# Optimization experiments

Hardware: AMD Instinct MI355X
Metric: run time of the kernel (lower is better)

The kernel has to match this reference:

```python
import jax, jax.numpy as jnp
from jax import lax
import numpy as np

T, B, D = 24, 64, 1536
R, NUM_BLOCK = 5120, 5
NBN = R // NUM_BLOCK  # 1024 neurons per block
C = 100
THR_BASE = 0.5
REF_BASE = 0.5
Q0 = 0.8  # (100-20)/100 from wta_mem_update


@jax.custom_vjp
def spike_fn(v):
    # act_fun: heaviside forward, rectangular surrogate gradient
    return (v > 0).astype(v.dtype)

def _spike_fwd(v):
    return (v > 0).astype(v.dtype), v

def _spike_bwd(v, g):
    return (g * (jnp.abs(v) < 0.5).astype(g.dtype),)

spike_fn.defvjp(_spike_fwd, _spike_bwd)


def setup_inputs() -> dict:
    key = jax.random.key(0)
    ks = jax.random.split(key, 16)
    f32 = jnp.float32
    x = jax.random.normal(ks[0], (T, B, D), dtype=f32)
    Wp = jax.random.normal(ks[1], (R, D), dtype=f32) / np.sqrt(D)
    Wl = jax.random.normal(ks[2], (R, R), dtype=f32) / np.sqrt(R)
    Wm = jax.random.normal(ks[3], (C, R), dtype=f32) / np.sqrt(R)
    # adaptive LIF per-neuron parameters (as in __init__)
    decay = jax.random.uniform(ks[4], (R,), dtype=f32)
    thr_beta = 0.1 * jax.random.uniform(ks[5], (R,), dtype=f32)
    thr_decay = 0.5 * jax.random.uniform(ks[6], (R,), dtype=f32)
    ref_beta = 0.1 * jax.random.uniform(ks[7], (R,), dtype=f32)
    ref_decay = 0.5 * jax.random.uniform(ks[8], (R,), dtype=f32)
    cur_beta = 0.1 * jax.random.uniform(ks[9], (R,), dtype=f32)
    cur_decay = 0.5 * jax.random.uniform(ks[10], (R,), dtype=f32)
    # block-structured projection mask: [D, R] then transpose to weight layout [R, D]
    mask = np.zeros((D, R), dtype=np.float32)
    cum = np.cumsum([0, 512, 512, 256, 128])  # [0,512,1024,1280,1408]
    for i in range(len(cum) - 1):
        mask[cum[i]:cum[i + 1], NBN * i:NBN * (i + 1)] = 1.0
    proj_mask = jnp.asarray(mask.T)
    # sparse lateral mask: rand>0.8, no self-connection
    rng = np.random.RandomState(0)
    lat = (rng.rand(R, R) > 0.8).astype(np.float32)
    lat = lat * (1.0 - np.eye(R, dtype=np.float32))
    lat_mask = jnp.asarray(lat.T)
    return {
        "x": x, "ln_g": jnp.ones((D,), f32), "ln_b": jnp.zeros((D,), f32),
        "Wp": Wp, "bp": jnp.zeros((R,), f32), "Wl": Wl, "bl": jnp.zeros((R,), f32),
        "Wm": Wm, "bm": jnp.zeros((C,), f32),
        "decay": decay, "thr_beta": thr_beta, "thr_decay": thr_decay,
        "ref_beta": ref_beta, "ref_decay": ref_decay,
        "cur_beta": cur_beta, "cur_decay": cur_decay,
        "proj_mask": proj_mask, "lat_mask": lat_mask,
    }


def reference(x, ln_g, ln_b, Wp, bp, Wl, bl, Wm, bm,
              decay, thr_beta, thr_decay, ref_beta, ref_decay,
              cur_beta, cur_decay, proj_mask, lat_mask):
    Tn, Bn, Dn = x.shape
    Rn = Wp.shape[0]
    # parameter clamps done in forward of the torch module
    dec = jnp.clip(decay, 0.0, 1.0)
    thd = jnp.clip(thr_decay, 0.0, 1.0)
    rfd = jnp.clip(ref_decay, 0.0, 1.0)
    cud = jnp.clip(cur_decay, 0.0, 1.0)
    Wp_m = Wp * proj_mask       # masked feedforward projection
    Wl_m = Wl * lat_mask        # masked lateral recurrence
    # LayerNorm over fused multimodal features
    mu = x.mean(-1, keepdims=True)
    var = x.var(-1, keepdims=True)
    xn = (x - mu) * lax.rsqrt(var + 1e-5) * ln_g + ln_b
    # precompute feedforward drive for all steps: [T, B, R]
    drive = jnp.einsum('tbd,rd->tbr', xn, Wp_m) + bp

    def step(carry, dr_t):
        spike, mem, ttr, rtr, ctr, ssum = carry
        state = dr_t + spike @ Wl_m.T + bl
        thr = THR_BASE + thr_beta * ttr
        ref = REF_BASE + ref_beta * rtr
        cur = cur_beta * ctr
        mem = (mem - spike * ref) * dec + state + cur
        # WTA: quantile-threshold per group (torch row-major reshape [B, NBN, NUM_BLOCK])
        m3 = mem.reshape(Bn, NBN, NUM_BLOCK)
        nps = jnp.quantile(m3, Q0, axis=1, keepdims=True)
        mem = jax.nn.relu(m3 - nps).reshape(Bn, Rn)
        spk = spike_fn(mem - thr)
        ttr = ttr * thd + spk
        rtr = rtr * rfd + spk
        ctr = ctr * cud + spk
        return (spk, mem, ttr, rtr, ctr, ssum + spk), None

    z = jnp.zeros((Bn, Rn), x.dtype)
    (spk, mem, _, _, _, ssum), _ = lax.scan(step, (z, z, z, z, z, z), drive)
    # readout on time-averaged spike counts
    return (ssum / Tn) @ Wm.T + bm
```

## Files before the change

### kernel.cpp

```cpp
#include <hip/hip_runtime.h>
#include <math.h>

#define TSTEPS 24
#define BB 64
#define DD 1536
#define RR 5120
#define NB 5
#define CC 100
#define KS 2
#define WSCALE 67108864.0f

typedef int i32x4 __attribute__((ext_vector_type(4)));

__device__ __forceinline__ int q_to_r(int q) { return (q & 1023) * 5 + (q >> 10); }

__constant__ int KOFF[4] = {0, 512, 1024, 1280};
__constant__ int KLEN[4] = {512, 512, 256, 128};
__constant__ int PBASE[4] = {0, 524288, 1048576, 1310720};

__device__ __forceinline__ unsigned fkey(float f) {
  unsigned u = __float_as_uint(f);
  return u ^ (((unsigned)((int)u >> 31)) | 0x80000000u);
}
__device__ __forceinline__ float fkeyinv(unsigned k) {
  unsigned u = (k & 0x80000000u) ? (k ^ 0x80000000u) : ~k;
  return __uint_as_float(u);
}

__global__ __launch_bounds__(256) void k_zero(float* __restrict__ state,
                                              unsigned* __restrict__ spike_i8_u32) {
  size_t n = 6ull * BB * RR;
  size_t nb = (size_t)BB * RR / 4;
  size_t gi = (size_t)blockIdx.x * 256 + threadIdx.x;
  for (size_t i = gi; i < n; i += (size_t)gridDim.x * 256) state[i] = 0.0f;
  for (size_t i = gi; i < nb; i += (size_t)gridDim.x * 256) spike_i8_u32[i] = 0u;
}

__global__ __launch_bounds__(256) void k_prep_params(
    const float* __restrict__ bp, const float* __restrict__ bl,
    const float* __restrict__ dec, const float* __restrict__ tb,
    const float* __restrict__ td, const float* __restrict__ rb,
    const float* __restrict__ rd, const float* __restrict__ cb,
    const float* __restrict__ cd, float* __restrict__ P) {
  int q = blockIdx.x * 256 + threadIdx.x;
  if (q >= RR) return;
  int r = q_to_r(q);
  P[0 * RR + q] = bp[r] + bl[r];
  P[1 * RR + q] = fminf(fmaxf(dec[r], 0.f), 1.f);
  P[2 * RR + q] = tb[r];
  P[3 * RR + q] = fminf(fmaxf(td[r], 0.f), 1.f);
  P[4 * RR + q] = rb[r];
  P[5 * RR + q] = fminf(fmaxf(rd[r], 0.f), 1.f);
  P[6 * RR + q] = cb[r];
  P[7 * RR + q] = fminf(fmaxf(cd[r], 0.f), 1.f);
}

__global__ __launch_bounds__(256) void k_prep_wm(const float* __restrict__ Wm,
                                                 float* __restrict__ Wmp) {
  int c = blockIdx.x;
  for (int q = threadIdx.x; q < RR; q += 256)
    Wmp[(size_t)c * RR + q] = Wm[(size_t)c * RR + q_to_r(q)];
}

__global__ __launch_bounds__(256) void k_prep_wpb(const float* __restrict__ Wp,
                                                  const float* __restrict__ pm,
                                                  float* __restrict__ Wpb) {
  int r = blockIdx.x;
  int i = r >> 10;
  int koff = KOFF[i], klen = KLEN[i];
  const float* src = Wp + (size_t)r * DD + koff;
  const float* msk = pm + (size_t)r * DD + koff;
  float* dst = Wpb + PBASE[i] + (size_t)(r - (i << 10)) * klen;
  for (int k = threadIdx.x; k < klen; k += 256) dst[k] = src[k] * msk[k];
}

__global__ __launch_bounds__(256) void k_build_q4tab(const float* __restrict__ bp,
                                                     const float* __restrict__ bl,
                                                     int* __restrict__ qtab,
                                                     float* __restrict__ vtab) {
  for (int idx = threadIdx.x; idx < 1024; idx += 256) {
    int j, i;
    if (idx < 204) { j = 0; i = 820 + idx; }
    else { int e = idx - 204; j = 1 + e / 205; i = 819 + e % 205; }
    int r = i * 5 + j;
    qtab[idx] = j * 1024 + i;
    vtab[idx] = bp[r] + bl[r];
  }
}

__global__ __launch_bounds__(256) void k_build_wq_i8(const float* __restrict__ Wl,
                                                     const float* __restrict__ lmask,
                                                     signed char* __restrict__ Bd) {
  int qn = blockIdx.x;
  int rn = q_to_r(qn);
  const float4* wr = (const float4*)(Wl + (size_t)rn * RR);
  const float4* mr = (const float4*)(lmask + (size_t)rn * RR);
  size_t ob = (size_t)qn * RR;
  const size_t plane = (size_t)RR * RR;
  for (int v4 = threadIdx.x; v4 < RR / 4; v4 += 256) {
    float4 wv = wr[v4];
    float4 mv = mr[v4];
    float w[4] = {wv.x * mv.x, wv.y * mv.y, wv.z * mv.z, wv.w * mv.w};
    unsigned char o0[4], o1[4], o2[4];
#pragma unroll
    for (int c = 0; c < 4; c++) {
      int wi = (int)rintf(w[c] * WSCALE);
      int d0 = (int)(signed char)(wi & 0xFF);
      int rem = (wi - d0) >> 8;
      int d1 = (int)(signed char)(rem & 0xFF);
      rem = (rem - d1) >> 8;
      o0[c] = (unsigned char)d0;
      o1[c] = (unsigned char)d1;
      o2[c] = (unsigned char)(rem & 0xFF);
    }
    *(uchar4*)(Bd + ob + 4 * v4) = make_uchar4(o0[0], o0[1], o0[2], o0[3]);
    *(uchar4*)(Bd + plane + ob + 4 * v4) = make_uchar4(o1[0], o1[1], o1[2], o1[3]);
    *(uchar4*)(Bd + 2 * plane + ob + 4 * v4) = make_uchar4(o2[0], o2[1], o2[2], o2[3]);
  }
}

__global__ __launch_bounds__(256) void k_layernorm(const float* __restrict__ x,
                                                   const float* __restrict__ g,
                                                   const float* __restrict__ be,
                                                   float* __restrict__ xn) {
  __shared__ float red[4];
  int row = blockIdx.x;
  int tid = threadIdx.x;
  const float* xr = x + (size_t)row * DD;
  float v[6];
  float s = 0.f;
#pragma unroll
  for (int i = 0; i < 6; i++) { v[i] = xr[i * 256 + tid]; s += v[i]; }
  for (int o = 32; o > 0; o >>= 1) s += __shfl_down(s, o, 64);
  int wv = tid >> 6, lane = tid & 63;
  if (lane == 0) red[wv] = s;
  __syncthreads();
  float mu = (red[0] + red[1] + red[2] + red[3]) * (1.0f / DD);
  __syncthreads();
  float sq = 0.f;
#pragma unroll
  for (int i = 0; i < 6; i++) { float d = v[i] - mu; sq += d * d; }
  for (int o = 32; o > 0; o >>= 1) sq += __shfl_down(sq, o, 64);
  if (lane == 0) red[wv] = sq;
  __syncthreads();
  float var = (red[0] + red[1] + red[2] + red[3]) * (1.0f / DD);
  float sc = 1.0f / sqrtf(var + 1e-5f);
#pragma unroll
  for (int i = 0; i < 6; i++) {
    int c = i * 256 + tid;
    xn[(size_t)row * DD + c] = (v[i] - mu) * sc * g[c] + be[c];
  }
}

__global__ __launch_bounds__(256) void k_gemm_drive(const float* __restrict__ A,
                                                    const float* __restrict__ Wpb,
                                                    const float* __restrict__ bp,
                                                    const float* __restrict__ bl,
                                                    float* __restrict__ Co) {
  __shared__ __align__(16) float As[16][68];
  __shared__ __align__(16) float Bs[16][68];
  int tid = threadIdx.x;
  int ib = blockIdx.z;
  int klen = KLEN[ib], koff = KOFF[ib];
  int m0 = blockIdx.y * 64;
  int n0t = blockIdx.x * 64;
  int lr = tid >> 2;
  int lq = tid & 3;
  int tx = tid & 15;
  int ty = tid >> 4;
  float acc[4][4] = {};
  const float4* Arow = (const float4*)(A + (size_t)(m0 + lr) * DD + koff);
  const float4* Brow = (const float4*)(Wpb + PBASE[ib] + (size_t)(n0t + lr) * klen);
  for (int k0 = 0; k0 < klen; k0 += 16) {
    float4 av = Arow[(k0 >> 2) + lq];
    float4 bv = Brow[(k0 >> 2) + lq];
    __syncthreads();
    As[lq * 4 + 0][lr] = av.x; As[lq * 4 + 1][lr] = av.y;
    As[lq * 4 + 2][lr] = av.z; As[lq * 4 + 3][lr] = av.w;
    Bs[lq * 4 + 0][lr] = bv.x; Bs[lq * 4 + 1][lr] = bv.y;
    Bs[lq * 4 + 2][lr] = bv.z; Bs[lq * 4 + 3][lr] = bv.w;
    __syncthreads();
#pragma unroll
    for (int kk = 0; kk < 16; kk++) {
      float4 a4 = *(const float4*)&As[kk][ty * 4];
      float4 b4 = *(const float4*)&Bs[kk][tx * 4];
      float av2[4] = {a4.x, a4.y, a4.z, a4.w};
      float bv2[4] = {b4.x, b4.y, b4.z, b4.w};
#pragma unroll
      for (int i2 = 0; i2 < 4; i2++)
#pragma unroll
        for (int j2 = 0; j2 < 4; j2++) acc[i2][j2] += av2[i2] * bv2[j2];
    }
  }
  int rbase = (ib << 10) + n0t + tx * 4;
  float bb[4];
  int qd[4];
#pragma unroll
  for (int j2 = 0; j2 < 4; j2++) {
    int rr = rbase + j2;
    bb[j2] = bp[rr] + bl[rr];
    qd[j2] = (rr % 5) * 1024 + rr / 5;
  }
#pragma unroll
  for (int i2 = 0; i2 < 4; i2++) {
    float* orow = Co + (size_t)(m0 + ty * 4 + i2) * RR;
#pragma unroll
    for (int j2 = 0; j2 < 4; j2++) orow[qd[j2]] = acc[i2][j2] + bb[j2];
  }
}

__global__ __launch_bounds__(256) void k_drive_fill4(const int* __restrict__ qtab,
                                                     const float* __restrict__ vtab,
                                                     float* __restrict__ drive) {
  int row = blockIdx.x;
  float* dr = drive + (size_t)row * RR;
  for (int k = threadIdx.x; k < 1024; k += 256) dr[qtab[k]] = vtab[k];
}

__global__ __launch_bounds__(256) void k_lat_gemm(const signed char* __restrict__ Asp,
                                                  const signed char* __restrict__ Bd,
                                                  long long* __restrict__ latp) {
  __shared__ long long lds[4][16][64];
  int tid = threadIdx.x;
  int lane = tid & 63;
  int w = tid >> 6;
  int n0 = blockIdx.x * 16;
  int ks = blockIdx.y;
  int k0 = ks * (RR / KS) + w * (RR / (KS * 4));
  int lm = lane & 15, lh = lane >> 4;
  const size_t plane = (size_t)RR * RR;
  i32x4 acc[4][3];
#pragma unroll
  for (int s = 0; s < 4; s++)
#pragma unroll
    for (int d = 0; d < 3; d++) acc[s][d] = (i32x4){0, 0, 0, 0};
  const i32x4* ap0 = (const i32x4*)(Asp + (size_t)(lm) * RR + k0 + lh * 16);
  const i32x4* ap1 = (const i32x4*)(Asp + (size_t)(16 + lm) * RR + k0 + lh * 16);
  const i32x4* ap2 = (const i32x4*)(Asp + (size_t)(32 + lm) * RR + k0 + lh * 16);
  const i32x4* ap3 = (const i32x4*)(Asp + (size_t)(48 + lm) * RR + k0 + lh * 16);
  const i32x4* bp0 = (const i32x4*)(Bd + (size_t)(n0 + lm) * RR + k0 + lh * 16);
  const i32x4* bp1 = (const i32x4*)(Bd + plane + (size_t)(n0 + lm) * RR + k0 + lh * 16);
  const i32x4* bp2 = (const i32x4*)(Bd + 2 * plane + (size_t)(n0 + lm) * RR + k0 + lh * 16);
#pragma unroll 2
  for (int kk = 0; kk < RR / (KS * 4 * 64); kk++) {
    i32x4 a0 = ap0[kk * 4];
    i32x4 a1 = ap1[kk * 4];
    i32x4 a2 = ap2[kk * 4];
    i32x4 a3 = ap3[kk * 4];
    i32x4 b0 = bp0[kk * 4];
    i32x4 b1 = bp1[kk * 4];
    i32x4 b2 = bp2[kk * 4];
    acc[0][0] = __builtin_amdgcn_mfma_i32_16x16x64_i8(a0, b0, acc[0][0], 0, 0, 0);
    acc[1][0] = __builtin_amdgcn_mfma_i32_16x16x64_i8(a1, b0, acc[1][0], 0, 0, 0);
    acc[2][0] = __builtin_amdgcn_mfma_i32_16x16x64_i8(a2, b0, acc[2][0], 0, 0, 0);
    acc[3][0] = __builtin_amdgcn_mfma_i32_16x16x64_i8(a3, b0, acc[3][0], 0, 0, 0);
    acc[0][1] = __builtin_amdgcn_mfma_i32_16x16x64_i8(a0, b1, acc[0][1], 0, 0, 0);
    acc[1][1] = __builtin_amdgcn_mfma_i32_16x16x64_i8(a1, b1, acc[1][1], 0, 0, 0);
    acc[2][1] = __builtin_amdgcn_mfma_i32_16x16x64_i8(a2, b1, acc[2][1], 0, 0, 0);
    acc[3][1] = __builtin_amdgcn_mfma_i32_16x16x64_i8(a3, b1, acc[3][1], 0, 0, 0);
    acc[0][2] = __builtin_amdgcn_mfma_i32_16x16x64_i8(a0, b2, acc[0][2], 0, 0, 0);
    acc[1][2] = __builtin_amdgcn_mfma_i32_16x16x64_i8(a1, b2, acc[1][2], 0, 0, 0);
    acc[2][2] = __builtin_amdgcn_mfma_i32_16x16x64_i8(a2, b2, acc[2][2], 0, 0, 0);
    acc[3][2] = __builtin_amdgcn_mfma_i32_16x16x64_i8(a3, b2, acc[3][2], 0, 0, 0);
  }
#pragma unroll
  for (int s = 0; s < 4; s++) {
#pragma unroll
    for (int r = 0; r < 4; r++) {
      long long v = (long long)acc[s][0][r]
                  + ((long long)acc[s][1][r] << 8)
                  + ((long long)acc[s][2][r] << 16);
      lds[w][s * 4 + r][lane] = v;
    }
  }
  __syncthreads();
  int o0 = tid * 4;
  int m = o0 >> 4;
  int ncb = o0 & 15;
  int s = m >> 4, lh2 = (m >> 2) & 3, rr = m & 3;
  long long* ob = latp + (size_t)ks * BB * RR + (size_t)m * RR + n0;
#pragma unroll
  for (int u = 0; u < 4; u++) {
    int nc = ncb + u;
    long long v = lds[0][s * 4 + rr][lh2 * 16 + nc]
                + lds[1][s * 4 + rr][lh2 * 16 + nc]
                + lds[2][s * 4 + rr][lh2 * 16 + nc]
                + lds[3][s * 4 + rr][lh2 * 16 + nc];
    ob[nc] = v;
  }
}

__global__ __launch_bounds__(256) void k_step(
    const float* __restrict__ drv_t,
    const long long* __restrict__ latp,
    const float* __restrict__ P,
    float* __restrict__ spike, float* __restrict__ memv,
    float* __restrict__ ttr, float* __restrict__ rtr, float* __restrict__ ctr,
    float* __restrict__ ssum, unsigned char* __restrict__ spike_i8) {
  __shared__ unsigned hist[256];
  __shared__ unsigned wtot[4];
  __shared__ unsigned s_prefix, s_rank, s_cle, s_min;

  int tid = threadIdx.x;
  int lane = tid & 63;
  int wv = tid >> 6;
  int j = blockIdx.x;
  int b = blockIdx.y;
  if (tid == 0) { s_prefix = 0u; s_rank = 818u; s_cle = 0u; s_min = 0xFFFFFFFFu; }

  size_t sbase = (size_t)b * RR + j * 1024 + 4 * tid;
  int pbase = j * 1024 + 4 * tid;
  long long li[4] = {0, 0, 0, 0};
#pragma unroll
  for (int ks = 0; ks < KS; ks++) {
    const long long* p = latp + (size_t)ks * BB * RR + sbase;
    li[0] += p[0]; li[1] += p[1]; li[2] += p[2]; li[3] += p[3];
  }
  float accf[4];
#pragma unroll
  for (int c = 0; c < 4; c++) accf[c] = (float)((double)li[c] * (1.0 / (double)WSCALE));

  float4 drv4 = *(const float4*)(drv_t + sbase);
  float4 mem4 = *(const float4*)(memv + sbase);
  float4 sp4 = *(const float4*)(spike + sbase);
  float4 tt4 = *(const float4*)(ttr + sbase);
  float4 tr4 = *(const float4*)(rtr + sbase);
  float4 tc4 = *(const float4*)(ctr + sbase);
  float4 dec4 = *(const float4*)(P + 1 * RR + pbase);
  float4 tb4 = *(const float4*)(P + 2 * RR + pbase);
  float4 rb4 = *(const float4*)(P + 4 * RR + pbase);
  float4 cb4 = *(const float4*)(P + 6 * RR + pbase);
  float mn[4], th[4];
  {
    const float* dv = (const float*)&drv4;
    const float* mv = (const float*)&mem4;
    const float* sv = (const float*)&sp4;
    const float* t1 = (const float*)&tt4;
    const float* t2 = (const float*)&tr4;
    const float* t3 = (const float*)&tc4;
    const float* dc = (const float*)&dec4;
    const float* b1 = (const float*)&tb4;
    const float* b2 = (const float*)&rb4;
    const float* b3 = (const float*)&cb4;
#pragma unroll
    for (int c = 0; c < 4; c++) {
      float rf = 0.5f + b2[c] * t2[c];
      float cu = b3[c] * t3[c];
      th[c] = 0.5f + b1[c] * t1[c];
      mn[c] = (mv[c] - sv[c] * rf) * dc[c] + (dv[c] + accf[c]) + cu;
    }
  }
  unsigned k4[4];
#pragma unroll
  for (int c = 0; c < 4; c++) k4[c] = fkey(mn[c]);

#pragma unroll
  for (int pass = 0; pass < 4; pass++) {
    int shift = 24 - pass * 8;
    unsigned maskhi = (pass == 0) ? 0u : (0xFFFFFFFFu << (shift + 8));
    hist[tid] = 0u;
    __syncthreads();
    unsigned pfx = s_prefix;
    unsigned rank = s_rank;
#pragma unroll
    for (int c = 0; c < 4; c++)
      if ((k4[c] & maskhi) == (pfx & maskhi)) atomicAdd(&hist[(k4[c] >> shift) & 255u], 1u);
    __syncthreads();
    unsigned cnt0 = hist[tid];
    unsigned v = cnt0;
    for (int o = 1; o < 64; o <<= 1) {
      unsigned n = (unsigned)__shfl_up((int)v, o, 64);
      if (lane >= o) v += n;
    }
    if (lane == 63) wtot[wv] = v;
    __syncthreads();
    unsigned add = 0;
    for (int w = 0; w < wv; w++) add += wtot[w];
    unsigned incl = v + add;
    unsigned excl = incl - cnt0;
    if (rank >= excl && rank < incl) {
      s_prefix = pfx | (((unsigned)tid) << shift);
      s_rank = rank - excl;
    }
    __syncthreads();
  }
  unsigned u818 = s_prefix;
  {
    int cl = 0;
    unsigned mnk = 0xFFFFFFFFu;
#pragma unroll
    for (int c = 0; c < 4; c++) {
      cl += (k4[c] <= u818) ? 1 : 0;
      if (k4[c] > u818) mnk = min(mnk, k4[c]);
    }
    atomicAdd(&s_cle, (unsigned)cl);
    atomicMin(&s_min, mnk);
  }
  __syncthreads();
  unsigned u819 = (s_cle >= 820u) ? u818 : s_min;
  float f818 = fkeyinv(u818), f819 = fkeyinv(u819);
  float nps = f818 + (0.8f * 1023.0f - 818.0f) * (f819 - f818);

  float4 td4 = *(const float4*)(P + 3 * RR + pbase);
  float4 rd4 = *(const float4*)(P + 5 * RR + pbase);
  float4 cd4 = *(const float4*)(P + 7 * RR + pbase);
  float4 ss4 = *(const float4*)(ssum + sbase);
  unsigned char si[4];
  {
    const float* d1 = (const float*)&td4;
    const float* d2 = (const float*)&rd4;
    const float* d3 = (const float*)&cd4;
    float* t1 = (float*)&tt4;
    float* t2 = (float*)&tr4;
    float* t3 = (float*)&tc4;
    float* sv = (float*)&sp4;
    float* mv = (float*)&mem4;
    float* ss = (float*)&ss4;
#pragma unroll
    for (int c = 0; c < 4; c++) {
      float mw = fmaxf(mn[c] - nps, 0.f);
      float sk = (mw - th[c] > 0.f) ? 1.f : 0.f;
      si[c] = (sk > 0.5f) ? (unsigned char)1 : (unsigned char)0;
      mv[c] = mw;
      t1[c] = t1[c] * d1[c] + sk;
      t2[c] = t2[c] * d2[c] + sk;
      t3[c] = t3[c] * d3[c] + sk;
      sv[c] = sk;
      ss[c] += sk;
    }
  }
  *(float4*)(memv + sbase) = mem4;
  *(float4*)(spike + sbase) = sp4;
  *(float4*)(ttr + sbase) = tt4;
  *(float4*)(rtr + sbase) = tr4;
  *(float4*)(ctr + sbase) = tc4;
  *(float4*)(ssum + sbase) = ss4;
  {
    unsigned char* sb8 = spike_i8 + (size_t)b * RR;
    int ibase = 4 * tid;
#pragma unroll
    for (int c = 0; c < 4; c++) sb8[(ibase + c) * 5 + j] = si[c];
  }
}

__global__ __launch_bounds__(256) void k_readout(const float* __restrict__ ssum,
                                                 const float* __restrict__ Wmp,
                                                 const float* __restrict__ bm,
                                                 float* __restrict__ out) {
  __shared__ float red[4];
  int c = blockIdx.x;
  int b = blockIdx.y;
  int tid = threadIdx.x;
  const float4* sp = (const float4*)(ssum + (size_t)b * RR);
  const float4* wp = (const float4*)(Wmp + (size_t)c * RR);
  float acc = 0.f;
#pragma unroll
  for (int i = 0; i < 5; i++) {
    float4 s4 = sp[i * 256 + tid];
    float4 w4 = wp[i * 256 + tid];
    acc += s4.x * w4.x + s4.y * w4.y + s4.z * w4.z + s4.w * w4.w;
  }
  for (int o = 32; o > 0; o >>= 1) acc += __shfl_down(acc, o, 64);
  if ((tid & 63) == 0) red[tid >> 6] = acc;
  __syncthreads();
  if (tid == 0)
    out[b * CC + c] = (red[0] + red[1] + red[2] + red[3]) * (1.0f / 24.0f) + bm[c];
}

extern "C" void kernel_launch(void* const* d_in, const int* in_sizes, int n_in,
                              void* d_out, int out_size, void* d_ws, size_t ws_size,
                              hipStream_t stream) {
  const float* x = (const float*)d_in[0];
  const float* ln_g = (const float*)d_in[1];
  const float* ln_b = (const float*)d_in[2];
  const float* Wp = (const float*)d_in[3];
  const float* bp = (const float*)d_in[4];
  const float* Wl = (const float*)d_in[5];
  const float* bl = (const float*)d_in[6];
  const float* Wm = (const float*)d_in[7];
  const float* bm = (const float*)d_in[8];
  const float* decay = (const float*)d_in[9];
  const float* thr_beta = (const float*)d_in[10];
  const float* thr_decay = (const float*)d_in[11];
  const float* ref_beta = (const float*)d_in[12];
  const float* ref_decay = (const float*)d_in[13];
  const float* cur_beta = (const float*)d_in[14];
  const float* cur_decay = (const float*)d_in[15];
  const float* proj_mask = (const float*)d_in[16];
  const float* lat_mask = (const float*)d_in[17];
  float* out = (float*)d_out;

  float* ws = (float*)d_ws;
  float* Wpb = ws;
  float* xn = Wpb + 1442 * 1024;
  float* drive = xn + (size_t)TSTEPS * BB * DD;
  float* state = drive + (size_t)TSTEPS * BB * RR;
  float* spike = state;
  float* memv = spike + (size_t)BB * RR;
  float* ttr = memv + (size_t)BB * RR;
  float* rtr = ttr + (size_t)BB * RR;
  float* ctr = rtr + (size_t)BB * RR;
  float* ssum = ctr + (size_t)BB * RR;
  float* P = ssum + (size_t)BB * RR;
  float* Wmp = P + 8 * RR;
  int* qtab = (int*)(Wmp + (size_t)CC * RR);
  float* vtab = (float*)(qtab + 1024);
  long long* latp = (long long*)(vtab + 1024 + 64);
  signed char* Bd = (signed char*)(latp + (size_t)KS * BB * RR);
  unsigned char* spike_i8 = (unsigned char*)(Bd + 3ull * RR * RR);

  hipLaunchKernelGGL(k_zero, dim3(512), dim3(256), 0, stream, state,
                     (unsigned*)spike_i8);
  hipLaunchKernelGGL(k_prep_params, dim3((RR + 255) / 256), dim3(256), 0, stream,
                     bp, bl, decay, thr_beta, thr_decay, ref_beta, ref_decay,
                     cur_beta, cur_decay, P);
  hipLaunchKernelGGL(k_prep_wm, dim3(CC), dim3(256), 0, stream, Wm, Wmp);
  hipLaunchKernelGGL(k_prep_wpb, dim3(4096), dim3(256), 0, stream, Wp, proj_mask, Wpb);
  hipLaunchKernelGGL(k_build_q4tab, dim3(1), dim3(256), 0, stream, bp, bl, qtab, vtab);
  hipLaunchKernelGGL(k_build_wq_i8, dim3(RR), dim3(256), 0, stream, Wl, lat_mask, Bd);
  hipLaunchKernelGGL(k_layernorm, dim3(TSTEPS * BB), dim3(256), 0, stream,
                     x, ln_g, ln_b, xn);
  hipLaunchKernelGGL(k_gemm_drive, dim3(16, (TSTEPS * BB) / 64, 4), dim3(256), 0,
                     stream, xn, Wpb, bp, bl, drive);
  hipLaunchKernelGGL(k_drive_fill4, dim3(TSTEPS * BB), dim3(256), 0, stream,
                     qtab, vtab, drive);
  for (int t = 0; t < TSTEPS; t++) {
    hipLaunchKernelGGL(k_lat_gemm, dim3(RR / 16, KS), dim3(256), 0, stream,
                       (const signed char*)spike_i8, Bd, latp);
    hipLaunchKernelGGL(k_step, dim3(NB, BB), dim3(256), 0, stream,
                       drive + (size_t)t * BB * RR, latp, P,
                       spike, memv, ttr, rtr, ctr, ssum, spike_i8);
  }
  hipLaunchKernelGGL(k_readout, dim3(CC, BB), dim3(256), 0, stream, ssum, Wmp, bm, out);
}
```

Baseline: 1.150 ms.

## Fuse lateral GEMM and neuron step into one kernel with atomic counter sync

The per-timestep int8 lateral GEMM and the LIF/WTA step kernel are merged into a single launch. Each GEMM block publishes its partial sums with agent-scope atomic stores and then increments a per-group counter. The ks=0 blocks then spin until all 128 contributing tiles for their neuron group have arrived, and run the step update for one batch row. Spike int8 buffers are double-buffered so the next step's input is not overwritten while other blocks still read it. This removes one kernel launch and its serialization per timestep. In exchange it adds a spin-wait that depends on enough blocks being co-resident on the device, plus atomic and polling overhead.

Measured after the change: 1.662 ms. 1.45x slower.

```diff
diff --git a/kernel.cpp b/kernel.cpp
--- a/kernel.cpp
+++ b/kernel.cpp
@@ -27,11 +27,20 @@
   return __uint_as_float(u);
 }
 
+__device__ __forceinline__ void astore64(long long* p_, long long v) {
+  __hip_atomic_store(p_, v, __ATOMIC_RELAXED, __HIP_MEMORY_SCOPE_AGENT);
+}
+__device__ __forceinline__ long long aload64(const long long* p_) {
+  return __hip_atomic_load(p_, __ATOMIC_RELAXED, __HIP_MEMORY_SCOPE_AGENT);
+}
+
 __global__ __launch_bounds__(256) void k_zero(float* __restrict__ state,
-                                              unsigned* __restrict__ spike_i8_u32) {
+                                              unsigned* __restrict__ spike_i8_u32,
+                                              unsigned* __restrict__ cnt) {
   size_t n = 6ull * BB * RR;
-  size_t nb = (size_t)BB * RR / 4;
+  size_t nb = 2ull * BB * RR / 4;
   size_t gi = (size_t)blockIdx.x * 256 + threadIdx.x;
+  if (gi < TSTEPS * NB * 16) cnt[gi] = 0u;
   for (size_t i = gi; i < n; i += (size_t)gridDim.x * 256) state[i] = 0.0f;
   for (size_t i = gi; i < nb; i += (size_t)gridDim.x * 256) spike_i8_u32[i] = 0u;
 }
@@ -217,104 +226,124 @@
   for (int k = threadIdx.x; k < 1024; k += 256) dr[qtab[k]] = vtab[k];
 }
 
-__global__ __launch_bounds__(256) void k_lat_gemm(const signed char* __restrict__ Asp,
-                                                  const signed char* __restrict__ Bd,
-                                                  long long* __restrict__ latp) {
+__global__ __launch_bounds__(256, 2) void k_fused(
+    const signed char* __restrict__ spike_in, const signed char* __restrict__ Bd,
+    long long* __restrict__ latp,
+    const float* __restrict__ drv_t, const float* __restrict__ P,
+    float* __restrict__ spike, float* __restrict__ memv,
+    float* __restrict__ ttr, float* __restrict__ rtr, float* __restrict__ ctr,
+    float* __restrict__ ssum, unsigned char* __restrict__ spike_out,
+    unsigned* __restrict__ cnt_t) {
   __shared__ long long lds[4][16][64];
+  __shared__ unsigned hist[256];
+  __shared__ unsigned wtot[4];
+  __shared__ unsigned scnt[16];
+  __shared__ unsigned s_prefix, s_rank, s_cle, s_min;
+
   int tid = threadIdx.x;
   int lane = tid & 63;
   int w = tid >> 6;
-  int n0 = blockIdx.x * 16;
+  int nt = blockIdx.x;
   int ks = blockIdx.y;
-  int k0 = ks * (RR / KS) + w * (RR / (KS * 4));
+  int n0 = nt * 16;
+  int jg = nt >> 6;
   int lm = lane & 15, lh = lane >> 4;
   const size_t plane = (size_t)RR * RR;
-  i32x4 acc[4][3];
-#pragma unroll
-  for (int s = 0; s < 4; s++)
-#pragma unroll
-    for (int d = 0; d < 3; d++) acc[s][d] = (i32x4){0, 0, 0, 0};
-  const i32x4* ap0 = (const i32x4*)(Asp + (size_t)(lm) * RR + k0 + lh * 16);
-  const i32x4* ap1 = (const i32x4*)(Asp + (size_t)(16 + lm) * RR + k0 + lh * 16);
-  const i32x4* ap2 = (const i32x4*)(Asp + (size_t)(32 + lm) * RR + k0 + lh * 16);
-  const i32x4* ap3 = (const i32x4*)(Asp + (size_t)(48 + lm) * RR + k0 + lh * 16);
-  const i32x4* bp0 = (const i32x4*)(Bd + (size_t)(n0 + lm) * RR + k0 + lh * 16);
-  const i32x4* bp1 = (const i32x4*)(Bd + plane + (size_t)(n0 + lm) * RR + k0 + lh * 16);
-  const i32x4* bp2 = (const i32x4*)(Bd + 2 * plane + (size_t)(n0 + lm) * RR + k0 + lh * 16);
+
+  {
+    int k0 = ks * (RR / KS) + w * (RR / (KS * 4));
+    i32x4 acc[4][3];
+#pragma unroll
+    for (int s = 0; s < 4; s++)
+#pragma unroll
+      for (int d = 0; d < 3; d++) acc[s][d] = (i32x4){0, 0, 0, 0};
+    const i32x4* ap0 = (const i32x4*)(spike_in + (size_t)(lm) * RR + k0 + lh * 16);
+    const i32x4* ap1 = (const i32x4*)(spike_in + (size_t)(16 + lm) * RR + k0 + lh * 16);
+    const i32x4* ap2 = (const i32x4*)(spike_in + (size_t)(32 + lm) * RR + k0 + lh * 16);
+    const i32x4* ap3 = (const i32x4*)(spike_in + (size_t)(48 + lm) * RR + k0 + lh * 16);
+    const i32x4* bp0 = (const i32x4*)(Bd + (size_t)(n0 + lm) * RR + k0 + lh * 16);
+    const i32x4* bp1 = (const i32x4*)(Bd + plane + (size_t)(n0 + lm) * RR + k0 + lh * 16);
+    const i32x4* bp2 = (const i32x4*)(Bd + 2 * plane + (size_t)(n0 + lm) * RR + k0 + lh * 16);
 #pragma unroll 2
-  for (int kk = 0; kk < RR / (KS * 4 * 64); kk++) {
-    i32x4 a0 = ap0[kk * 4];
-    i32x4 a1 = ap1[kk * 4];
-    i32x4 a2 = ap2[kk * 4];
-    i32x4 a3 = ap3[kk * 4];
-    i32x4 b0 = bp0[kk * 4];
-    i32x4 b1 = bp1[kk * 4];
-    i32x4 b2 = bp2[kk * 4];
-    acc[0][0] = __builtin_amdgcn_mfma_i32_16x16x64_i8(a0, b0, acc[0][0], 0, 0, 0);
-    acc[1][0] = __builtin_amdgcn_mfma_i32_16x16x64_i8(a1, b0, acc[1][0], 0, 0, 0);
-    acc[2][0] = __builtin_amdgcn_mfma_i32_16x16x64_i8(a2, b0, acc[2][0], 0, 0, 0);
-    acc[3][0] = __builtin_amdgcn_mfma_i32_16x16x64_i8(a3, b0, acc[3][0], 0, 0, 0);
-    acc[0][1] = __builtin_amdgcn_mfma_i32_16x16x64_i8(a0, b1, acc[0][1], 0, 0, 0);
-    acc[1][1] = __builtin_amdgcn_mfma_i32_16x16x64_i8(a1, b1, acc[1][1], 0, 0, 0);
-    acc[2][1] = __builtin_amdgcn_mfma_i32_16x16x64_i8(a2, b1, acc[2][1], 0, 0, 0);
-    acc[3][1] = __builtin_amdgcn_mfma_i32_16x16x64_i8(a3, b1, acc[3][1], 0, 0, 0);
-    acc[0][2] = __builtin_amdgcn_mfma_i32_16x16x64_i8(a0, b2, acc[0][2], 0, 0, 0);
-    acc[1][2] = __builtin_amdgcn_mfma_i32_16x16x64_i8(a1, b2, acc[1][2], 0, 0, 0);
-    acc[2][2] = __builtin_amdgcn_mfma_i32_16x16x64_i8(a2, b2, acc[2][2], 0, 0, 0);
-    acc[3][2] = __builtin_amdgcn_mfma_i32_16x16x64_i8(a3, b2, acc[3][2], 0, 0, 0);
-  }
-#pragma unroll
-  for (int s = 0; s < 4; s++) {
-#pragma unroll
-    for (int r = 0; r < 4; r++) {
-      long long v = (long long)acc[s][0][r]
-                  + ((long long)acc[s][1][r] << 8)
-                  + ((long long)acc[s][2][r] << 16);
-      lds[w][s * 4 + r][lane] = v;
-    }
-  }
+    for (int kk = 0; kk < RR / (KS * 4 * 64); kk++) {
+      i32x4 a0 = ap0[kk * 4];
+      i32x4 a1 = ap1[kk * 4];
+      i32x4 a2 = ap2[kk * 4];
+      i32x4 a3 = ap3[kk * 4];
+      i32x4 b0 = bp0[kk * 4];
+      i32x4 b1 = bp1[kk * 4];
+      i32x4 b2 = bp2[kk * 4];
+      acc[0][0] = __builtin_amdgcn_mfma_i32_16x16x64_i8(a0, b0, acc[0][0], 0, 0, 0);
+      acc[1][0] = __builtin_amdgcn_mfma_i32_16x16x64_i8(a1, b0, acc[1][0], 0, 0, 0);
+      acc[2][0] = __builtin_amdgcn_mfma_i32_16x16x64_i8(a2, b0, acc[2][0], 0, 0, 0);
+      acc[3][0] = __builtin_amdgcn_mfma_i32_16x16x64_i8(a3, b0, acc[3][0], 0, 0, 0);
+      acc[0][1] = __builtin_amdgcn_mfma_i32_16x16x64_i8(a0, b1, acc[0][1], 0, 0, 0);
+      acc[1][1] = __builtin_amdgcn_mfma_i32_16x16x64_i8(a1, b1, acc[1][1], 0, 0, 0);
+      acc[2][1] = __builtin_amdgcn_mfma_i32_16x16x64_i8(a2, b1, acc[2][1], 0, 0, 0);
+      acc[3][1] = __builtin_amdgcn_mfma_i32_16x16x64_i8(a3, b1, acc[3][1], 0, 0, 0);
+      acc[0][2] = __builtin_amdgcn_mfma_i32_16x16x64_i8(a0, b2, acc[0][2], 0, 0, 0);
+      acc[1][2] = __builtin_amdgcn_mfma_i32_16x16x64_i8(a1, b2, acc[1][2], 0, 0, 0);
+      acc[2][2] = __builtin_amdgcn_mfma_i32_16x16x64_i8(a2, b2, acc[2][2], 0, 0, 0);
+      acc[3][2] = __builtin_amdgcn_mfma_i32_16x16x64_i8(a3, b2, acc[3][2], 0, 0, 0);
+    }
+#pragma unroll
+    for (int s = 0; s < 4; s++) {
+#pragma unroll
+      for (int r = 0; r < 4; r++) {
+        long long v = (long long)acc[s][0][r]
+                    + ((long long)acc[s][1][r] << 8)
+                    + ((long long)acc[s][2][r] << 16);
+        lds[w][s * 4 + r][lane] = v;
+      }
+    }
+    __syncthreads();
+    int o0 = tid * 4;
+    int m = o0 >> 4;
+    int ncb = o0 & 15;
+    int s = m >> 4, lh2 = (m >> 2) & 3, rr = m & 3;
+    long long* ob = latp + (size_t)ks * BB * RR + (size_t)m * RR + n0;
+#pragma unroll
+    for (int u = 0; u < 4; u++) {
+      int nc = ncb + u;
+      long long v = lds[0][s * 4 + rr][lh2 * 16 + nc]
+                  + lds[1][s * 4 + rr][lh2 * 16 + nc]
+                  + lds[2][s * 4 + rr][lh2 * 16 + nc]
+                  + lds[3][s * 4 + rr][lh2 * 16 + nc];
+      astore64(ob + nc, v);
+    }
+  }
+  asm volatile("s_waitcnt vmcnt(0)" ::: "memory");
   __syncthreads();
-  int o0 = tid * 4;
-  int m = o0 >> 4;
-  int ncb = o0 & 15;
-  int s = m >> 4, lh2 = (m >> 2) & 3, rr = m & 3;
-  long long* ob = latp + (size_t)ks * BB * RR + (size_t)m * RR + n0;
-#pragma unroll
-  for (int u = 0; u < 4; u++) {
-    int nc = ncb + u;
-    long long v = lds[0][s * 4 + rr][lh2 * 16 + nc]
-                + lds[1][s * 4 + rr][lh2 * 16 + nc]
-                + lds[2][s * 4 + rr][lh2 * 16 + nc]
-                + lds[3][s * 4 + rr][lh2 * 16 + nc];
-    ob[nc] = v;
-  }
-}
-
-__global__ __launch_bounds__(256) void k_step(
-    const float* __restrict__ drv_t,
-    const long long* __restrict__ latp,
-    const float* __restrict__ P,
-    float* __restrict__ spike, float* __restrict__ memv,
-    float* __restrict__ ttr, float* __restrict__ rtr, float* __restrict__ ctr,
-    float* __restrict__ ssum, unsigned char* __restrict__ spike_i8) {
-  __shared__ unsigned hist[256];
-  __shared__ unsigned wtot[4];
-  __shared__ unsigned s_prefix, s_rank, s_cle, s_min;
-
-  int tid = threadIdx.x;
-  int lane = tid & 63;
-  int wv = tid >> 6;
-  int j = blockIdx.x;
-  int b = blockIdx.y;
+  if (tid == 0)
+    __hip_atomic_fetch_add(&cnt_t[jg * 16 + (nt & 15)], 1u,
+                           __ATOMIC_RELAXED, __HIP_MEMORY_SCOPE_AGENT);
+  if (ks == 1) return;
+
+  int b = nt & 63;
+  {
+    unsigned s;
+    do {
+      __syncthreads();
+      if (tid < 16)
+        scnt[tid] = __hip_atomic_load(&cnt_t[jg * 16 + tid], __ATOMIC_RELAXED,
+                                      __HIP_MEMORY_SCOPE_AGENT);
+      __syncthreads();
+      s = 0;
+#pragma unroll
+      for (int i = 0; i < 16; i++) s += scnt[i];
+      if (s < 128u) __builtin_amdgcn_s_sleep(16);
+    } while (s < 128u);
+  }
   if (tid == 0) { s_prefix = 0u; s_rank = 818u; s_cle = 0u; s_min = 0xFFFFFFFFu; }
 
-  size_t sbase = (size_t)b * RR + j * 1024 + 4 * tid;
-  int pbase = j * 1024 + 4 * tid;
+  size_t sbase = (size_t)b * RR + jg * 1024 + 4 * tid;
+  int pbase = jg * 1024 + 4 * tid;
   long long li[4] = {0, 0, 0, 0};
 #pragma unroll
-  for (int ks = 0; ks < KS; ks++) {
-    const long long* p = latp + (size_t)ks * BB * RR + sbase;
-    li[0] += p[0]; li[1] += p[1]; li[2] += p[2]; li[3] += p[3];
+  for (int kss = 0; kss < KS; kss++) {
+    const long long* p = latp + (size_t)kss * BB * RR + sbase;
+#pragma unroll
+    for (int c = 0; c < 4; c++) li[c] += aload64(p + c);
   }
   float accf[4];
 #pragma unroll
@@ -372,10 +401,10 @@
       unsigned n = (unsigned)__shfl_up((int)v, o, 64);
       if (lane >= o) v += n;
     }
-    if (lane == 63) wtot[wv] = v;
+    if (lane == 63) wtot[w] = v;
     __syncthreads();
     unsigned add = 0;
-    for (int w = 0; w < wv; w++) add += wtot[w];
+    for (int ww = 0; ww < w; ww++) add += wtot[ww];
     unsigned incl = v + add;
     unsigned excl = incl - cnt0;
     if (rank >= excl && rank < incl) {
@@ -436,10 +465,10 @@
   *(float4*)(ctr + sbase) = tc4;
   *(float4*)(ssum + sbase) = ss4;
   {
-    unsigned char* sb8 = spike_i8 + (size_t)b * RR;
+    unsigned char* sb8 = spike_out + (size_t)b * RR;
     int ibase = 4 * tid;
 #pragma unroll
-    for (int c = 0; c < 4; c++) sb8[(ibase + c) * 5 + j] = si[c];
+    for (int c = 0; c < 4; c++) sb8[(ibase + c) * 5 + jg] = si[c];
   }
 }
 
@@ -505,12 +534,13 @@
   float* Wmp = P + 8 * RR;
   int* qtab = (int*)(Wmp + (size_t)CC * RR);
   float* vtab = (float*)(qtab + 1024);
-  long long* latp = (long long*)(vtab + 1024 + 64);
+  unsigned* cnt = (unsigned*)(vtab + 1024);
+  long long* latp = (long long*)(cnt + TSTEPS * NB * 16 + 64);
   signed char* Bd = (signed char*)(latp + (size_t)KS * BB * RR);
   unsigned char* spike_i8 = (unsigned char*)(Bd + 3ull * RR * RR);
 
   hipLaunchKernelGGL(k_zero, dim3(512), dim3(256), 0, stream, state,
-                     (unsigned*)spike_i8);
+                     (unsigned*)spike_i8, cnt);
   hipLaunchKernelGGL(k_prep_params, dim3((RR + 255) / 256), dim3(256), 0, stream,
                      bp, bl, decay, thr_beta, thr_decay, ref_beta, ref_decay,
                      cur_beta, cur_decay, P);
@@ -525,11 +555,13 @@
   hipLaunchKernelGGL(k_drive_fill4, dim3(TSTEPS * BB), dim3(256), 0, stream,
                      qtab, vtab, drive);
   for (int t = 0; t < TSTEPS; t++) {
-    hipLaunchKernelGGL(k_lat_gemm, dim3(RR / 16, KS), dim3(256), 0, stream,
-                       (const signed char*)spike_i8, Bd, latp);
-    hipLaunchKernelGGL(k_step, dim3(NB, BB), dim3(256), 0, stream,
-                       drive + (size_t)t * BB * RR, latp, P,
-                       spike, memv, ttr, rtr, ctr, ssum, spike_i8);
+    unsigned char* sin = spike_i8 + (size_t)(t & 1) * BB * RR;
+    unsigned char* sout = spike_i8 + (size_t)((t + 1) & 1) * BB * RR;
+    hipLaunchKernelGGL(k_fused, dim3(RR / 16, KS), dim3(256), 0, stream,
+                       (const signed char*)sin, Bd, latp,
+                       drive + (size_t)t * BB * RR, P,
+                       spike, memv, ttr, rtr, ctr, ssum, sout,
+                       cnt + t * NB * 16);
   }
   hipLaunchKernelGGL(k_readout, dim3(CC, BB), dim3(256), 0, stream, ssum, Wmp, bm, out);
 }
```
